# Kernel tuning notes

Measured on AMD Instinct MI355X. Metric: run time of the kernel, lower is better.

Reference implementation:

```python
import jax, jax.numpy as jnp
import numpy as np

# Multi-scale ball-query config (PFE.SA_LAYER.raw_points)
RADII = (0.8, 1.6)
NSAMPLES = (16, 32)
PC_SCALE = jnp.array([40.0, 40.0, 4.0])  # spread points over a realistic lidar extent


def _fps(pts, num_keypoints):
    """Furthest point sampling. pts: [N,3] -> idx [K] (int32). First pick = 0."""
    n = pts.shape[0]

    def step(carry, _):
        dists, last = carry
        d = jnp.sum((pts - pts[last]) ** 2, axis=-1)
        dists = jnp.minimum(dists, d)
        nxt = jnp.argmax(dists).astype(jnp.int32)
        return (dists, nxt), last

    init = (jnp.full((n,), 1e10, pts.dtype), jnp.int32(0))
    _, idxs = jax.lax.scan(step, init, None, length=num_keypoints)
    return idxs


def _glorot(k, shape):
    return jax.random.normal(k, shape) * (2.0 / (shape[0] + shape[1])) ** 0.5


def setup_inputs() -> dict:
    key = jax.random.key(0)
    ks = jax.random.split(key, 8)
    B, N = 2, 16384
    xyz = jax.random.uniform(ks[0], (B, N, 3)) * PC_SCALE          # [B,N,3]
    feat = jax.random.normal(ks[1], (B, 1, N))                      # intensity channel
    clouds = jnp.concatenate([xyz.transpose(0, 2, 1), feat], axis=1)  # [B,4,N]
    return {
        "clouds": clouds,
        "w1_a": _glorot(ks[2], (4, 128)),
        "w2_a": _glorot(ks[3], (128, 256)),
        "w1_b": _glorot(ks[4], (4, 128)),
        "w2_b": _glorot(ks[5], (128, 256)),
        "w_fuse": _glorot(ks[6], (512, 128)),
        "num_keypoints": 4096,
    }


def reference(clouds, w1_a, w2_a, w1_b, w2_b, w_fuse, num_keypoints):
    # clouds: [B, 4, N] with channels [x, y, z, intensity]
    xyz = clouds[:, :3, :].transpose(0, 2, 1)    # [B,N,3]
    feats = clouds[:, 3:, :].transpose(0, 2, 1)  # [B,N,1]

    # --- FPS keypoint sampling (per cloud) ---
    kp_idx = jax.vmap(lambda p: _fps(p, num_keypoints))(xyz)             # [B,K]
    keypoints = jnp.take_along_axis(xyz, kp_idx[:, :, None], axis=1)     # [B,K,3]

    # --- pairwise squared distances keypoints->points, shared by all scales ---
    d2 = jnp.sum((keypoints[:, :, None, :] - xyz[:, None, :, :]) ** 2, axis=-1)  # [B,K,N]

    gather = jax.vmap(lambda x, i: x[i])  # [N,C],[K,ns] -> [K,ns,C]

    pooled = []
    for r, ns, W1, W2 in ((RADII[0], NSAMPLES[0], w1_a, w2_a),
                          (RADII[1], NSAMPLES[1], w1_b, w2_b)):
        neg, idx = jax.lax.top_k(-d2, ns)            # ns nearest neighbors
        valid = (-neg) < (r * r)                     # [B,K,ns] within ball radius
        g_xyz = gather(xyz, idx) - keypoints[:, :, None, :]   # [B,K,ns,3] relative coords
        g_f = gather(feats, idx)                              # [B,K,ns,1]
        g = jnp.concatenate([g_xyz, g_f], axis=-1)            # [B,K,ns,4] (use_xyz=True)
        h = jax.nn.relu(jax.nn.relu(g @ W1) @ W2)             # shared PointNet MLP
        h = jnp.where(valid[..., None], h, 0.0)               # mask out-of-ball (relu>=0)
        pooled.append(jnp.max(h, axis=2))                     # max_pool -> [B,K,256]

    fused = jax.nn.relu(jnp.concatenate(pooled, axis=-1) @ w_fuse)  # [B,K,128]
    return jnp.concatenate([keypoints, fused], axis=-1)             # [B,K,3+128]
```

## Files before the change

### kernel.cpp

```cpp
#include <hip/hip_runtime.h>

typedef unsigned int u32;
typedef unsigned long long u64;
typedef float v2f __attribute__((ext_vector_type(2)));

__device__ __forceinline__ u64 shflx64(u64 v, int m) {
  int lo = __shfl_xor((int)(u32)v, m, 64);
  int hi = __shfl_xor((int)(u32)(v >> 32), m, 64);
  return ((u64)(u32)hi << 32) | (u32)lo;
}
__device__ __forceinline__ u64 maxu64(u64 a, u64 b) { return a > b ? a : b; }

template <int CTRL>
__device__ __forceinline__ u64 dpp_max64(u64 k) {
  int slo = __builtin_amdgcn_update_dpp(0, (int)(u32)k, CTRL, 0xF, 0xF, true);
  int shi = __builtin_amdgcn_update_dpp(0, (int)(u32)(k >> 32), CTRL, 0xF, 0xF, true);
  u64 s = ((u64)(u32)shi << 32) | (u32)slo;
  return maxu64(k, s);
}

__device__ __forceinline__ u64 row_max64(u64 k) {
  k = dpp_max64<0xB1>(k);
  k = dpp_max64<0x4E>(k);
  k = dpp_max64<0x124>(k);
  k = dpp_max64<0x128>(k);
  return k;
}

__device__ __forceinline__ float boxlb(float cx, float cy, float cz,
                                       float nx, float xx, float ny, float xy,
                                       float nz, float xz) {
  float gx = fmaxf(fmaxf(nx - cx, cx - xx), 0.0f);
  float gy = fmaxf(fmaxf(ny - cy, cy - xy), 0.0f);
  float gz = fmaxf(fmaxf(nz - cz, cz - xz), 0.0f);
  return gx * gx + gy * gy + gz * gz;
}

#define SORT_T 1024

__global__ __launch_bounds__(SORT_T) void k_sort(const float* __restrict__ clouds,
                                                 u32* __restrict__ order,
                                                 u32* __restrict__ bends,
                                                 float* __restrict__ meta, int N) {
  const int b = blockIdx.x, tid = threadIdx.x;
  const float* xs = clouds + (size_t)b * 4 * N;
  const float* ys = xs + N;
  const float* zs = ys + N;

  __shared__ u32 hist[2048];
  __shared__ u32 base[2048];
  __shared__ float red[96];
  __shared__ u32 wsum[16];

  float mnx = 3.4e38f, mxx = -3.4e38f, mny = 3.4e38f, mxy = -3.4e38f,
        mnz = 3.4e38f, mxz = -3.4e38f;
  for (int i = tid; i < N; i += SORT_T) {
    float x = xs[i], y = ys[i], z = zs[i];
    mnx = fminf(mnx, x); mxx = fmaxf(mxx, x);
    mny = fminf(mny, y); mxy = fmaxf(mxy, y);
    mnz = fminf(mnz, z); mxz = fmaxf(mxz, z);
  }
#pragma unroll
  for (int s = 1; s < 64; s <<= 1) {
    mnx = fminf(mnx, __shfl_xor(mnx, s, 64)); mxx = fmaxf(mxx, __shfl_xor(mxx, s, 64));
    mny = fminf(mny, __shfl_xor(mny, s, 64)); mxy = fmaxf(mxy, __shfl_xor(mxy, s, 64));
    mnz = fminf(mnz, __shfl_xor(mnz, s, 64)); mxz = fmaxf(mxz, __shfl_xor(mxz, s, 64));
  }
  const int wv = tid >> 6, ln = tid & 63;
  if (ln == 0) {
    red[wv * 6 + 0] = mnx; red[wv * 6 + 1] = mxx;
    red[wv * 6 + 2] = mny; red[wv * 6 + 3] = mxy;
    red[wv * 6 + 4] = mnz; red[wv * 6 + 5] = mxz;
  }
  hist[tid] = 0u; hist[tid + 1024] = 0u;
  __syncthreads();
  float bmnx = red[0], bmxx = red[1], bmny = red[2], bmxy = red[3],
        bmnz = red[4], bmxz = red[5];
// ... 35 lines not shown
  for (int d = 1; d < 64; d <<= 1) {
    u32 o = (u32)__shfl_up((int)x, d, 64);
    if (ln >= d) x += o;
  }
  if (ln == 63) wsum[wv] = x;
  __syncthreads();
  u32 wpre = 0;
#pragma unroll
  for (int w = 0; w < 16; ++w) wpre += (w < wv) ? wsum[w] : 0u;
  u32 tbase = wpre + x - ts;
  base[2 * tid] = tbase;
  base[2 * tid + 1] = tbase + s0;
  __syncthreads();

  for (int i = tid; i < N; i += SORT_T) {
    int qx = min(15, max(0, (int)((xs[i] - bmnx) * sx)));
    int qy = min(15, max(0, (int)((ys[i] - bmny) * sy)));
    int qz = min(7, max(0, (int)((zs[i] - bmnz) * sz)));
    u32 m = 0; int sh = 0;
#pragma unroll
    for (int bit = 0; bit < 4; ++bit) {
      m |= ((u32)((qx >> bit) & 1)) << sh++;
      m |= ((u32)((qy >> bit) & 1)) << sh++;
      if (bit < 3) m |= ((u32)((qz >> bit) & 1)) << sh++;
    }
    u32 pos = atomicAdd(&base[m], 1u);
    order[(size_t)b * N + pos] = (u32)i;
  }
  __syncthreads();
  for (int m = tid; m < 2048; m += SORT_T)
    bends[(size_t)b * 2048 + m] = base[m];
}

#define FPS_T 1024

__global__ __launch_bounds__(FPS_T, 4) void k_fps(const float* __restrict__ clouds,
                                                  const u32* __restrict__ order,
                                                  float* __restrict__ keyp,
                                                  int N, int K) {
  const int b = blockIdx.x, tid = threadIdx.x;
  const float* xs = clouds + (size_t)b * 4 * N;
  const float* ys = xs + N;
  const float* zs = ys + N;

  int oid[16];
  v2f px2[8], py2[8], pz2[8], dd2[8];
#pragma unroll
  for (int j = 0; j < 16; ++j) oid[j] = (int)order[(size_t)b * N + tid * 16 + j];
#pragma unroll
  for (int i = 0; i < 8; ++i) {
    px2[i].x = xs[oid[2 * i]]; px2[i].y = xs[oid[2 * i + 1]];
    py2[i].x = ys[oid[2 * i]]; py2[i].y = ys[oid[2 * i + 1]];
    pz2[i].x = zs[oid[2 * i]]; pz2[i].y = zs[oid[2 * i + 1]];
    dd2[i].x = 1e10f; dd2[i].y = 1e10f;
  }
  float bnx = px2[0].x, bxx = px2[0].x, bny = py2[0].x, bxy = py2[0].x,
        bnz = pz2[0].x, bxz = pz2[0].x;
#pragma unroll
  for (int i = 0; i < 8; ++i) {
    bnx = fminf(bnx, fminf(px2[i].x, px2[i].y));
    bxx = fmaxf(bxx, fmaxf(px2[i].x, px2[i].y));
    bny = fminf(bny, fminf(py2[i].x, py2[i].y));
    bxy = fmaxf(bxy, fmaxf(py2[i].x, py2[i].y));
    bnz = fminf(bnz, fminf(pz2[i].x, pz2[i].y));
    bxz = fmaxf(bxz, fmaxf(pz2[i].x, pz2[i].y));
  }
  float rnx = bnx, rxx = bxx, rny = bny, rxy = bxy, rnz = bnz, rxz = bxz;
#pragma unroll
  for (int s = 1; s < 16; s <<= 1) {
    rnx = fminf(rnx, __shfl_xor(rnx, s, 64)); rxx = fmaxf(rxx, __shfl_xor(rxx, s, 64));
    rny = fminf(rny, __shfl_xor(rny, s, 64)); rxy = fmaxf(rxy, __shfl_xor(rxy, s, 64));
    rnz = fminf(rnz, __shfl_xor(rnz, s, 64)); rxz = fmaxf(rxz, __shfl_xor(rxz, s, 64));
  }

  __shared__ u64 slots[2][64];
  const int wv = tid >> 6, ln = tid & 63;
  const int row = wv * 4 + (ln >> 4);
  const int q = ln & 15;

  u64 ckey = 0, rkey = 0;
  float cmax = 1e10f, rmax = 1e10f;
  float cx = xs[0], cy = ys[0], cz = zs[0];
  if (tid == 0) {
    float* kb = keyp + (size_t)b * K * 3;
    kb[0] = cx; kb[1] = cy; kb[2] = cz;
  }

  for (int t = 1; t < K; ++t) {
    const int par = t & 1;
    float gx = fmaxf(fmaxf(rnx - cx, cx - rxx), 0.0f);
    float gy = fmaxf(fmaxf(rny - cy, cy - rxy), 0.0f);
    float gz = fmaxf(fmaxf(rnz - cz, cz - rxz), 0.0f);
    float lbr = gx * gx + gy * gy + gz * gz;
    if (lbr <= rmax * 1.00001f) {
      float hx = fmaxf(fmaxf(bnx - cx, cx - bxx), 0.0f);
      float hy = fmaxf(fmaxf(bny - cy, cy - bxy), 0.0f);
      float hz = fmaxf(fmaxf(bnz - cz, cz - bxz), 0.0f);
      float lbt = hx * hx + hy * hy + hz * hz;
      if (lbt <= cmax * 1.00001f) {
        v2f m2 = {0.0f, 0.0f};
        {
#pragma clang fp contract(off)
          const v2f c2x = {cx, cx}, c2y = {cy, cy}, c2z = {cz, cz};
#pragma unroll
          for (int i = 0; i < 8; ++i) {
            v2f dx = px2[i] - c2x;
            v2f dy = py2[i] - c2y;
            v2f dz = pz2[i] - c2z;
            v2f d = (dx * dx + dy * dy) + dz * dz;
            v2f nm = __builtin_elementwise_min(dd2[i], d);
            dd2[i] = nm;
            m2 = __builtin_elementwise_max(m2, nm);
          }
        }
        const float m = fmaxf(m2.x, m2.y);
        u32 mi = 0xFFFFFFFFu;
#pragma unroll
        for (int i = 0; i < 8; ++i) {
          if (dd2[i].x == m) mi = min(mi, (u32)oid[2 * i]);
          if (dd2[i].y == m) mi = min(mi, (u32)oid[2 * i + 1]);
        }
        cmax = m;
        ckey = ((u64)__float_as_uint(m) << 32) | (u64)(u32)(~mi);
      }
      rkey = row_max64(ckey);
      rmax = __uint_as_float((u32)(rkey >> 32));
    }
    if (q == 0) slots[par][row] = rkey;
    __syncthreads();
    u64 k0 = slots[par][q];
    u64 k1 = slots[par][q + 16];
    u64 k2 = slots[par][q + 32];
    u64 k3 = slots[par][q + 48];
    u64 g = maxu64(maxu64(k0, k1), maxu64(k2, k3));
    g = row_max64(g);
    const u32 widx = __builtin_amdgcn_readfirstlane(~(u32)g);
    cx = xs[widx]; cy = ys[widx]; cz = zs[widx];
    if (tid == 0) {
      float* kb = keyp + ((size_t)b * K + t) * 3;
      kb[0] = cx; kb[1] = cy; kb[2] = cz;
    }
  }
}

#define KNN_T 256
#define KNN_CAP 1024
#define SENTINEL (((u64)0x7F7FFFFFu) << 32)

__global__ __launch_bounds__(KNN_T) void k_knn(const float* __restrict__ clouds,
                                               const float* __restrict__ keyp,
                                               const u32* __restrict__ order,
                                               const u32* __restrict__ bends,
                                               const float* __restrict__ meta,
                                               u64* __restrict__ slots,
                                               float* __restrict__ out,
                                               int N, int K, float r2b) {
  const int kp = blockIdx.x;
  const int b = kp / K;
  const int tid = threadIdx.x;
  const float* xs = clouds + (size_t)b * 4 * N;
  const float* ys = xs + N;
  const float* zs = ys + N;

  __shared__ u64 cand[KNN_CAP];
  __shared__ u32 lends[2048];
  __shared__ u32 blist[2048];
  __shared__ int cnt, bcnt;
  __shared__ u64 sorted32[32];

  if (tid == 0) { cnt = 0; bcnt = 0; }
  if (tid < 32) sorted32[tid] = SENTINEL;
  for (int m = tid; m < 2048; m += KNN_T) lends[m] = bends[(size_t)b * 2048 + m];
  const float kx = keyp[(size_t)kp * 3 + 0];
  const float ky = keyp[(size_t)kp * 3 + 1];
  const float kz = keyp[(size_t)kp * 3 + 2];
  const float bmnx = meta[b * 8 + 0], bmny = meta[b * 8 + 1], bmnz = meta[b * 8 + 2];
  const float csx = meta[b * 8 + 3], csy = meta[b * 8 + 4], csz = meta[b * 8 + 5];
  __syncthreads();

  for (int m = tid; m < 2048; m += KNN_T) {
    u32 qx = (m & 1) | ((m >> 2) & 2) | ((m >> 4) & 4) | ((m >> 6) & 8);
    u32 qy = ((m >> 1) & 1) | ((m >> 3) & 2) | ((m >> 5) & 4) | ((m >> 7) & 8);
    u32 qz = ((m >> 2) & 1) | ((m >> 4) & 2) | ((m >> 6) & 4);
    float lx = bmnx + (float)qx * csx - 1e-3f, hx = bmnx + (float)(qx + 1) * csx + 1e-3f;
    float ly = bmny + (float)qy * csy - 1e-3f, hy = bmny + (float)(qy + 1) * csy + 1e-3f;
    float lz = bmnz + (float)qz * csz - 1e-3f, hz = bmnz + (float)(qz + 1) * csz + 1e-3f;
    if (boxlb(kx, ky, kz, lx, hx, ly, hy, lz, hz) < r2b) {
      u32 s = m ? lends[m - 1] : 0u;
      u32 e = lends[m];
      if (e > s) {
        int p = atomicAdd(&bcnt, 1);
        blist[p] = s | (e << 16);
      }
    }
  }
  __syncthreads();

  const int nb = bcnt;
  for (int bi = 0; bi < nb; ++bi) {
    u32 pk = blist[bi];
    u32 s = pk & 0xFFFFu, e = pk >> 16;
    for (u32 i = s + tid; i < e; i += KNN_T) {
      u32 pi = order[(size_t)b * N + i];
      float dx = __fsub_rn(xs[pi], kx), dy = __fsub_rn(ys[pi], ky),
            dz = __fsub_rn(zs[pi], kz);
      float d = __fadd_rn(__fadd_rn(__fmul_rn(dx, dx), __fmul_rn(dy, dy)),
                          __fmul_rn(dz, dz));
      if (d < r2b) {
        int p = atomicAdd(&cnt, 1);
        if (p < KNN_CAP)
          cand[p] = (((u64)__float_as_uint(d)) << 32) | (u64)pi;
      }
    }
  }
  __syncthreads();
  int n = min(cnt, KNN_CAP);
  for (int i = tid; i < n; i += KNN_T) {
    u64 kk = cand[i];
    int r = 0;
    for (int j = 0; j < n; ++j) r += (cand[j] < kk) ? 1 : 0;
    if (r < 32) sorted32[r] = kk;
  }
  __syncthreads();
  if (tid < 32) slots[(size_t)kp * 32 + tid] = sorted32[tid];
  if (tid < 3) out[(size_t)kp * 131 + tid] = keyp[(size_t)kp * 3 + tid];
}

template <int M>
__global__ __launch_bounds__(256) void k_pool(const float* __restrict__ clouds,
                                              const float* __restrict__ keyp,
                                              const u64* __restrict__ slots,
                                              const float* __restrict__ w1,
                                              const float* __restrict__ w2,
                                              float* __restrict__ pooled,
                                              int N, int K, float R2, int colOff) {
  constexpr int R = M / 4;
  const int kp = blockIdx.x;
  const int b = kp / K;
  const int tid = threadIdx.x;
  const float* xs = clouds + (size_t)b * 4 * N;
  const float* ys = xs + N;
  const float* zs = ys + N;
  const float* fs = zs + N;

  __shared__ float w1l[512];
  __shared__ float gx[32], gy[32], gz[32], gf[32];
  __shared__ float h1l[32 * 132];
  __shared__ float w2l[32 * 256];
  __shared__ u32 pm[256];

  const float kx = keyp[(size_t)kp * 3 + 0];
  const float ky = keyp[(size_t)kp * 3 + 1];
  const float kz = keyp[(size_t)kp * 3 + 2];

  w1l[tid] = w1[tid];
  w1l[tid + 256] = w1[tid + 256];
  pm[tid] = 0u;
  if (tid < M) {
    u64 sl = slots[(size_t)kp * 32 + tid];
    float d2 = __uint_as_float((u32)(sl >> 32));
    u32 idx = (u32)sl;
    float vx = 0.f, vy = 0.f, vz = 0.f, vf = 0.f;
    if (d2 < R2) {
      vx = xs[idx] - kx;
      vy = ys[idx] - ky;
      vz = zs[idx] - kz;
      vf = fs[idx];
    }
    gx[tid] = vx; gy[tid] = vy; gz[tid] = vz; gf[tid] = vf;
  }
  __syncthreads();

  {
    const int c = tid & 127;
#pragma unroll
    for (int p = 0; p < M / 2; ++p) {
      int r = p * 2 + (tid >> 7);
      float h = fmaf(gf[r], w1l[384 + c],
                fmaf(gz[r], w1l[256 + c],
                fmaf(gy[r], w1l[128 + c], gx[r] * w1l[c])));
      h1l[r * 132 + c] = fmaxf(h, 0.0f);
    }
  }

  const int rt = tid >> 6;
  const int cg = tid & 63;
  float acc[R][4];
#pragma unroll
  for (int rr = 0; rr < R; ++rr)
#pragma unroll
    for (int cc = 0; cc < 4; ++cc) acc[rr][cc] = 0.0f;

  for (int kt = 0; kt < 4; ++kt) {
    __syncthreads();
    for (int q = tid; q < 32 * 256; q += 256)
      w2l[q] = w2[(size_t)(kt * 32 + (q >> 8)) * 256 + (q & 255)];
    __syncthreads();
    for (int k = 0; k < 32; k += 4) {
      float4 hv[R];
#pragma unroll
      for (int rr = 0; rr < R; ++rr)
        hv[rr] = *reinterpret_cast<const float4*>(
            &h1l[(rt * R + rr) * 132 + kt * 32 + k]);
      float4 wv[4];
#pragma unroll
      for (int kk = 0; kk < 4; ++kk)
        wv[kk] = *reinterpret_cast<const float4*>(
            &w2l[(k + kk) * 256 + cg * 4]);
#pragma unroll
      for (int rr = 0; rr < R; ++rr) {
        const float a0 = hv[rr].x, a1 = hv[rr].y, a2 = hv[rr].z, a3 = hv[rr].w;
        acc[rr][0] = fmaf(a3, wv[3].x, fmaf(a2, wv[2].x,
                     fmaf(a1, wv[1].x, fmaf(a0, wv[0].x, acc[rr][0]))));
        acc[rr][1] = fmaf(a3, wv[3].y, fmaf(a2, wv[2].y,
                     fmaf(a1, wv[1].y, fmaf(a0, wv[0].y, acc[rr][1]))));
        acc[rr][2] = fmaf(a3, wv[3].z, fmaf(a2, wv[2].z,
                     fmaf(a1, wv[1].z, fmaf(a0, wv[0].z, acc[rr][2]))));
        acc[rr][3] = fmaf(a3, wv[3].w, fmaf(a2, wv[2].w,
                     fmaf(a1, wv[1].w, fmaf(a0, wv[0].w, acc[rr][3]))));
      }
    }
  }
#pragma unroll
  for (int cc = 0; cc < 4; ++cc) {
    float mx = 0.0f;
#pragma unroll
    for (int rr = 0; rr < R; ++rr) mx = fmaxf(mx, acc[rr][cc]);
    atomicMax(&pm[cg * 4 + cc], __float_as_uint(mx));
  }
  __syncthreads();
  pooled[(size_t)kp * 512 + colOff + tid] = __uint_as_float(pm[tid]);
}

__global__ __launch_bounds__(256) void k_fuse(const float* __restrict__ pooled,
                                              const float* __restrict__ wf,
                                              float* __restrict__ out) {
  const int m0 = blockIdx.x * 16;
  const int tid = threadIdx.x;
  __shared__ float al[16 * 516];
  __shared__ float wl[32 * 128];

  for (int q = tid; q < 16 * 512; q += 256)
    al[(q >> 9) * 516 + (q & 511)] =
        pooled[(size_t)(m0 + (q >> 9)) * 512 + (q & 511)];

  const int rg = tid >> 5;
  const int cg = tid & 31;
  float acc[2][4];
#pragma unroll
  for (int rr = 0; rr < 2; ++rr)
#pragma unroll
    for (int cc = 0; cc < 4; ++cc) acc[rr][cc] = 0.0f;

  for (int kt = 0; kt < 16; ++kt) {
    __syncthreads();
    for (int q = tid; q < 32 * 128; q += 256)
      wl[q] = wf[(size_t)(kt * 32 + (q >> 7)) * 128 + (q & 127)];
    __syncthreads();
    for (int k = 0; k < 32; k += 4) {
      float4 av[2];
#pragma unroll
      for (int rr = 0; rr < 2; ++rr)
        av[rr] = *reinterpret_cast<const float4*>(
            &al[(rg * 2 + rr) * 516 + kt * 32 + k]);
// ... 22 lines not shown
    for (int cc = 0; cc < 4; ++cc)
      out[row * 131 + 3 + cg * 4 + cc] = fmaxf(acc[rr][cc], 0.0f);
  }
}

extern "C" void kernel_launch(void* const* d_in, const int* in_sizes, int n_in,
                              void* d_out, int out_size, void* d_ws, size_t ws_size,
                              hipStream_t stream) {
  const float* clouds = (const float*)d_in[0];
  const float* w1a = (const float*)d_in[1];
  const float* w2a = (const float*)d_in[2];
  const float* w1b = (const float*)d_in[3];
  const float* w2b = (const float*)d_in[4];
  const float* wfu = (const float*)d_in[5];
  float* out = (float*)d_out;

  const int B = 2;
  const int N = in_sizes[0] / (4 * B);
  const int K = out_size / (131 * B);
  const int BK = B * K;

  char* ws = (char*)d_ws;
  u32* order = (u32*)ws;
  size_t off = ((size_t)B * N * sizeof(u32) + 255) & ~(size_t)255;
  u32* bends = (u32*)(ws + off);
  off += (size_t)B * 2048 * sizeof(u32);
  off = (off + 255) & ~(size_t)255;
  float* meta = (float*)(ws + off);
  off += (size_t)B * 8 * sizeof(float);
  off = (off + 255) & ~(size_t)255;
  float* keyp = (float*)(ws + off);
  off += (size_t)BK * 3 * sizeof(float);
  off = (off + 255) & ~(size_t)255;
  u64* slots = (u64*)(ws + off);
  off += (size_t)BK * 32 * sizeof(u64);
  off = (off + 255) & ~(size_t)255;
  float* pooled = (float*)(ws + off);

  const float r2a = (float)(0.8 * 0.8);
  const float r2b = (float)(1.6 * 1.6);

  k_sort<<<dim3(B), dim3(SORT_T), 0, stream>>>(clouds, order, bends, meta, N);
  k_fps<<<dim3(B), dim3(FPS_T), 0, stream>>>(clouds, order, keyp, N, K);
  k_knn<<<dim3(BK), dim3(KNN_T), 0, stream>>>(clouds, keyp, order, bends, meta,
                                              slots, out, N, K, r2b);
  k_pool<16><<<dim3(BK), dim3(256), 0, stream>>>(clouds, keyp, slots, w1a, w2a,
                                                 pooled, N, K, r2a, 0);
  k_pool<32><<<dim3(BK), dim3(256), 0, stream>>>(clouds, keyp, slots, w1b, w2b,
                                                 pooled, N, K, r2b, 256);
  k_fuse<<<dim3(BK / 16), dim3(256), 0, stream>>>(pooled, wfu, out);
}
```

Measured before the change: 4.400 ms.

## Overlap FPS with KNN and pooling in a persistent megakernel with progress flags

FPS, KNN and both pooling stages now run in one persistent kernel. Two blocks run FPS and publish keypoints in batches of 64 along with a per-cloud progress counter. The other blocks pull chunks of keypoints through an atomic work counter, spin until each keypoint is published, then run ball-query KNN and both PointNet MLPs back to back in shared memory. This hides the sequential FPS latency behind the downstream work and removes the intermediate slots buffer and two launches. The costs are spin-wait polling, co-residency assumptions for the FPS blocks, and 1024-thread worker blocks where many threads sit idle in the 256-wide MLP stages.

```diff
diff --git a/kernel.cpp b/kernel.cpp
--- a/kernel.cpp
+++ b/kernel.cpp
@@ -4,11 +4,6 @@
 typedef unsigned long long u64;
 typedef float v2f __attribute__((ext_vector_type(2)));
 
-__device__ __forceinline__ u64 shflx64(u64 v, int m) {
-  int lo = __shfl_xor((int)(u32)v, m, 64);
-  int hi = __shfl_xor((int)(u32)(v >> 32), m, 64);
-  return ((u64)(u32)hi << 32) | (u32)lo;
-}
 __device__ __forceinline__ u64 maxu64(u64 a, u64 b) { return a > b ? a : b; }
 
 template <int CTRL>
@@ -18,7 +13,6 @@
   u64 s = ((u64)(u32)shi << 32) | (u32)slo;
   return maxu64(k, s);
 }
-
 __device__ __forceinline__ u64 row_max64(u64 k) {
   k = dpp_max64<0xB1>(k);
   k = dpp_max64<0x4E>(k);
@@ -41,8 +35,10 @@
 __global__ __launch_bounds__(SORT_T) void k_sort(const float* __restrict__ clouds,
                                                  u32* __restrict__ order,
                                                  u32* __restrict__ bends,
-                                                 float* __restrict__ meta, int N) {
+                                                 float* __restrict__ meta,
+                                                 u32* prog, int N) {
   const int b = blockIdx.x, tid = threadIdx.x;
+  if (b == 0 && tid == 0) { prog[0] = 0u; prog[1] = 0u; prog[2] = 0u; }
   const float* xs = clouds + (size_t)b * 4 * N;
   const float* ys = xs + N;
   const float* zs = ys + N;
@@ -144,12 +140,16 @@
     bends[(size_t)b * 2048 + m] = base[m];
 }
 
-#define FPS_T 1024
-
-__global__ __launch_bounds__(FPS_T, 4) void k_fps(const float* __restrict__ clouds,
-                                                  const u32* __restrict__ order,
-                                                  float* __restrict__ keyp,
-                                                  int N, int K) {
+#define KNN_CAP 1024
+#define SENTINEL (((u64)0x7F7FFFFFu) << 32)
+#define CHUNK 4
+#define MEGA_T 1024
+
+#define SM_BYTES 37376
+
+__device__ void fps_body(const float* __restrict__ clouds,
+                         const u32* __restrict__ order,
+                         float* keyp, u32* prog, int N, int K, char* smemc) {
   const int b = blockIdx.x, tid = threadIdx.x;
   const float* xs = clouds + (size_t)b * 4 * N;
   const float* ys = xs + N;
@@ -185,7 +185,7 @@
     rnz = fminf(rnz, __shfl_xor(rnz, s, 64)); rxz = fmaxf(rxz, __shfl_xor(rxz, s, 64));
   }
 
-  __shared__ u64 slots[2][64];
+  u64 (*slots)[64] = (u64 (*)[64])smemc;
   const int wv = tid >> 6, ln = tid & 63;
   const int row = wv * 4 + (ln >> 4);
   const int q = ln & 15;
@@ -193,10 +193,7 @@
   u64 ckey = 0, rkey = 0;
   float cmax = 1e10f, rmax = 1e10f;
   float cx = xs[0], cy = ys[0], cz = zs[0];
-  if (tid == 0) {
-    float* kb = keyp + (size_t)b * K * 3;
-    kb[0] = cx; kb[1] = cy; kb[2] = cz;
-  }
+  float bpx = cx, bpy = cy, bpz = cz;
 
   for (int t = 1; t < K; ++t) {
     const int par = t & 1;
@@ -248,128 +245,48 @@
     g = row_max64(g);
     const u32 widx = __builtin_amdgcn_readfirstlane(~(u32)g);
     cx = xs[widx]; cy = ys[widx]; cz = zs[widx];
-    if (tid == 0) {
-      float* kb = keyp + ((size_t)b * K + t) * 3;
-      kb[0] = cx; kb[1] = cy; kb[2] = cz;
-    }
-  }
-}
-
-#define KNN_T 256
-#define KNN_CAP 1024
-#define SENTINEL (((u64)0x7F7FFFFFu) << 32)
-
-__global__ __launch_bounds__(KNN_T) void k_knn(const float* __restrict__ clouds,
-                                               const float* __restrict__ keyp,
-                                               const u32* __restrict__ order,
-                                               const u32* __restrict__ bends,
-                                               const float* __restrict__ meta,
-                                               u64* __restrict__ slots,
-                                               float* __restrict__ out,
-                                               int N, int K, float r2b) {
-  const int kp = blockIdx.x;
-  const int b = kp / K;
-  const int tid = threadIdx.x;
-  const float* xs = clouds + (size_t)b * 4 * N;
-  const float* ys = xs + N;
-  const float* zs = ys + N;
-
-  __shared__ u64 cand[KNN_CAP];
-  __shared__ u32 lends[2048];
-  __shared__ u32 blist[2048];
-  __shared__ int cnt, bcnt;
-  __shared__ u64 sorted32[32];
-
-  if (tid == 0) { cnt = 0; bcnt = 0; }
-  if (tid < 32) sorted32[tid] = SENTINEL;
-  for (int m = tid; m < 2048; m += KNN_T) lends[m] = bends[(size_t)b * 2048 + m];
-  const float kx = keyp[(size_t)kp * 3 + 0];
-  const float ky = keyp[(size_t)kp * 3 + 1];
-  const float kz = keyp[(size_t)kp * 3 + 2];
-  const float bmnx = meta[b * 8 + 0], bmny = meta[b * 8 + 1], bmnz = meta[b * 8 + 2];
-  const float csx = meta[b * 8 + 3], csy = meta[b * 8 + 4], csz = meta[b * 8 + 5];
-  __syncthreads();
-
-  for (int m = tid; m < 2048; m += KNN_T) {
-    u32 qx = (m & 1) | ((m >> 2) & 2) | ((m >> 4) & 4) | ((m >> 6) & 8);
-    u32 qy = ((m >> 1) & 1) | ((m >> 3) & 2) | ((m >> 5) & 4) | ((m >> 7) & 8);
-    u32 qz = ((m >> 2) & 1) | ((m >> 4) & 2) | ((m >> 6) & 4);
-    float lx = bmnx + (float)qx * csx - 1e-3f, hx = bmnx + (float)(qx + 1) * csx + 1e-3f;
-    float ly = bmny + (float)qy * csy - 1e-3f, hy = bmny + (float)(qy + 1) * csy + 1e-3f;
-    float lz = bmnz + (float)qz * csz - 1e-3f, hz = bmnz + (float)(qz + 1) * csz + 1e-3f;
-    if (boxlb(kx, ky, kz, lx, hx, ly, hy, lz, hz) < r2b) {
-      u32 s = m ? lends[m - 1] : 0u;
-      u32 e = lends[m];
-      if (e > s) {
-        int p = atomicAdd(&bcnt, 1);
-        blist[p] = s | (e << 16);
-      }
-    }
-  }
-  __syncthreads();
-
-  const int nb = bcnt;
-  for (int bi = 0; bi < nb; ++bi) {
-    u32 pk = blist[bi];
-    u32 s = pk & 0xFFFFu, e = pk >> 16;
-    for (u32 i = s + tid; i < e; i += KNN_T) {
-      u32 pi = order[(size_t)b * N + i];
-      float dx = __fsub_rn(xs[pi], kx), dy = __fsub_rn(ys[pi], ky),
-            dz = __fsub_rn(zs[pi], kz);
-      float d = __fadd_rn(__fadd_rn(__fmul_rn(dx, dx), __fmul_rn(dy, dy)),
-                          __fmul_rn(dz, dz));
-      if (d < r2b) {
-        int p = atomicAdd(&cnt, 1);
-        if (p < KNN_CAP)
-          cand[p] = (((u64)__float_as_uint(d)) << 32) | (u64)pi;
-      }
-    }
-  }
-  __syncthreads();
-  int n = min(cnt, KNN_CAP);
-  for (int i = tid; i < n; i += KNN_T) {
-    u64 kk = cand[i];
-    int r = 0;
-    for (int j = 0; j < n; ++j) r += (cand[j] < kk) ? 1 : 0;
-    if (r < 32) sorted32[r] = kk;
-  }
-  __syncthreads();
-  if (tid < 32) slots[(size_t)kp * 32 + tid] = sorted32[tid];
-  if (tid < 3) out[(size_t)kp * 131 + tid] = keyp[(size_t)kp * 3 + tid];
+    if (wv == 0) {
+      if (ln == (t & 63)) { bpx = cx; bpy = cy; bpz = cz; }
+      if ((t & 63) == 63) {
+        u32* kb = (u32*)keyp + ((size_t)b * K + (size_t)(t - 63 + ln)) * 3;
+        __hip_atomic_store(kb + 0, __float_as_uint(bpx), __ATOMIC_RELAXED, __HIP_MEMORY_SCOPE_AGENT);
+        __hip_atomic_store(kb + 1, __float_as_uint(bpy), __ATOMIC_RELAXED, __HIP_MEMORY_SCOPE_AGENT);
+        __hip_atomic_store(kb + 2, __float_as_uint(bpz), __ATOMIC_RELAXED, __HIP_MEMORY_SCOPE_AGENT);
+        asm volatile("s_waitcnt vmcnt(0)" ::: "memory");
+        if (ln == 0)
+          __hip_atomic_store(prog + b, (u32)(t + 1), __ATOMIC_RELAXED, __HIP_MEMORY_SCOPE_AGENT);
+      }
+    }
+  }
+  if ((K & 63) != 0 && wv == 0) {
+    int base = (K - 1) & ~63;
+    int kpt = base + ln;
+    if (kpt < K && ln <= ((K - 1) & 63)) {
+      u32* kb = (u32*)keyp + ((size_t)b * K + (size_t)kpt) * 3;
+      __hip_atomic_store(kb + 0, __float_as_uint(bpx), __ATOMIC_RELAXED, __HIP_MEMORY_SCOPE_AGENT);
+      __hip_atomic_store(kb + 1, __float_as_uint(bpy), __ATOMIC_RELAXED, __HIP_MEMORY_SCOPE_AGENT);
+      __hip_atomic_store(kb + 2, __float_as_uint(bpz), __ATOMIC_RELAXED, __HIP_MEMORY_SCOPE_AGENT);
+    }
+    asm volatile("s_waitcnt vmcnt(0)" ::: "memory");
+    if (ln == 0)
+      __hip_atomic_store(prog + b, (u32)K, __ATOMIC_RELAXED, __HIP_MEMORY_SCOPE_AGENT);
+  }
 }
 
 template <int M>
-__global__ __launch_bounds__(256) void k_pool(const float* __restrict__ clouds,
-                                              const float* __restrict__ keyp,
-                                              const u64* __restrict__ slots,
-                                              const float* __restrict__ w1,
-                                              const float* __restrict__ w2,
-                                              float* __restrict__ pooled,
-                                              int N, int K, float R2, int colOff) {
+__device__ void pool_stage(const float* xs, const float* ys, const float* zs,
+                           const float* fs, float kx, float ky, float kz,
+                           const u64* s32, const float* __restrict__ w1,
+                           const float* __restrict__ w2, float* pooled, int kp,
+                           float R2, int colOff, float* w1l, float* gxa,
+                           float* gya, float* gza, float* gfa, float* h1l,
+                           float* w2l, u32* pm, int tid) {
   constexpr int R = M / 4;
-  const int kp = blockIdx.x;
-  const int b = kp / K;
-  const int tid = threadIdx.x;
-  const float* xs = clouds + (size_t)b * 4 * N;
-  const float* ys = xs + N;
-  const float* zs = ys + N;
-  const float* fs = zs + N;
-
-  __shared__ float w1l[512];
-  __shared__ float gx[32], gy[32], gz[32], gf[32];
-  __shared__ float h1l[32 * 132];
-  __shared__ float w2l[32 * 256];
-  __shared__ u32 pm[256];
-
-  const float kx = keyp[(size_t)kp * 3 + 0];
-  const float ky = keyp[(size_t)kp * 3 + 1];
-  const float kz = keyp[(size_t)kp * 3 + 2];
-
-  w1l[tid] = w1[tid];
-  w1l[tid + 256] = w1[tid + 256];
-  pm[tid] = 0u;
+  __syncthreads();
+  if (tid < 512) w1l[tid] = w1[tid];
+  if (tid < 256) pm[tid] = 0u;
   if (tid < M) {
-    u64 sl = slots[(size_t)kp * 32 + tid];
+    u64 sl = s32[tid];
     float d2 = __uint_as_float((u32)(sl >> 32));
     u32 idx = (u32)sl;
     float vx = 0.f, vy = 0.f, vz = 0.f, vf = 0.f;
@@ -379,23 +296,23 @@
       vz = zs[idx] - kz;
       vf = fs[idx];
     }
-    gx[tid] = vx; gy[tid] = vy; gz[tid] = vz; gf[tid] = vf;
-  }
-  __syncthreads();
-
-  {
+    gxa[tid] = vx; gya[tid] = vy; gza[tid] = vz; gfa[tid] = vf;
+  }
+  __syncthreads();
+
+  if (tid < 256) {
     const int c = tid & 127;
 #pragma unroll
     for (int p = 0; p < M / 2; ++p) {
       int r = p * 2 + (tid >> 7);
-      float h = fmaf(gf[r], w1l[384 + c],
-                fmaf(gz[r], w1l[256 + c],
-                fmaf(gy[r], w1l[128 + c], gx[r] * w1l[c])));
+      float h = fmaf(gfa[r], w1l[384 + c],
+                fmaf(gza[r], w1l[256 + c],
+                fmaf(gya[r], w1l[128 + c], gxa[r] * w1l[c])));
       h1l[r * 132 + c] = fmaxf(h, 0.0f);
     }
   }
 
-  const int rt = tid >> 6;
+  const int rt = (tid & 255) >> 6;
   const int cg = tid & 63;
   float acc[R][4];
 #pragma unroll
@@ -403,45 +320,177 @@
 #pragma unroll
     for (int cc = 0; cc < 4; ++cc) acc[rr][cc] = 0.0f;
 
-  for (int kt = 0; kt < 4; ++kt) {
+  for (int kt = 0; kt < 8; ++kt) {
     __syncthreads();
-    for (int q = tid; q < 32 * 256; q += 256)
-      w2l[q] = w2[(size_t)(kt * 32 + (q >> 8)) * 256 + (q & 255)];
+    for (int q2 = tid; q2 < 16 * 256; q2 += MEGA_T)
+      w2l[q2] = w2[(size_t)(kt * 16 + (q2 >> 8)) * 256 + (q2 & 255)];
     __syncthreads();
-    for (int k = 0; k < 32; k += 4) {
-      float4 hv[R];
-#pragma unroll
-      for (int rr = 0; rr < R; ++rr)
-        hv[rr] = *reinterpret_cast<const float4*>(
-            &h1l[(rt * R + rr) * 132 + kt * 32 + k]);
-      float4 wv[4];
-#pragma unroll
-      for (int kk = 0; kk < 4; ++kk)
-        wv[kk] = *reinterpret_cast<const float4*>(
-            &w2l[(k + kk) * 256 + cg * 4]);
-#pragma unroll
-      for (int rr = 0; rr < R; ++rr) {
-        const float a0 = hv[rr].x, a1 = hv[rr].y, a2 = hv[rr].z, a3 = hv[rr].w;
-        acc[rr][0] = fmaf(a3, wv[3].x, fmaf(a2, wv[2].x,
-                     fmaf(a1, wv[1].x, fmaf(a0, wv[0].x, acc[rr][0]))));
-        acc[rr][1] = fmaf(a3, wv[3].y, fmaf(a2, wv[2].y,
-                     fmaf(a1, wv[1].y, fmaf(a0, wv[0].y, acc[rr][1]))));
-        acc[rr][2] = fmaf(a3, wv[3].z, fmaf(a2, wv[2].z,
-                     fmaf(a1, wv[1].z, fmaf(a0, wv[0].z, acc[rr][2]))));
-        acc[rr][3] = fmaf(a3, wv[3].w, fmaf(a2, wv[2].w,
-                     fmaf(a1, wv[1].w, fmaf(a0, wv[0].w, acc[rr][3]))));
-      }
-    }
-  }
-#pragma unroll
-  for (int cc = 0; cc < 4; ++cc) {
-    float mx = 0.0f;
-#pragma unroll
-    for (int rr = 0; rr < R; ++rr) mx = fmaxf(mx, acc[rr][cc]);
-    atomicMax(&pm[cg * 4 + cc], __float_as_uint(mx));
-  }
-  __syncthreads();
-  pooled[(size_t)kp * 512 + colOff + tid] = __uint_as_float(pm[tid]);
+    if (tid < 256) {
+      for (int k = 0; k < 16; k += 4) {
+        float4 hv[R];
+#pragma unroll
+        for (int rr = 0; rr < R; ++rr)
+          hv[rr] = *reinterpret_cast<const float4*>(
+              &h1l[(rt * R + rr) * 132 + kt * 16 + k]);
+        float4 wv[4];
+#pragma unroll
+        for (int kk = 0; kk < 4; ++kk)
+          wv[kk] = *reinterpret_cast<const float4*>(
+              &w2l[(k + kk) * 256 + cg * 4]);
+#pragma unroll
+        for (int rr = 0; rr < R; ++rr) {
+          const float a0 = hv[rr].x, a1 = hv[rr].y, a2 = hv[rr].z, a3 = hv[rr].w;
+          acc[rr][0] = fmaf(a3, wv[3].x, fmaf(a2, wv[2].x,
+                       fmaf(a1, wv[1].x, fmaf(a0, wv[0].x, acc[rr][0]))));
+          acc[rr][1] = fmaf(a3, wv[3].y, fmaf(a2, wv[2].y,
+                       fmaf(a1, wv[1].y, fmaf(a0, wv[0].y, acc[rr][1]))));
+          acc[rr][2] = fmaf(a3, wv[3].z, fmaf(a2, wv[2].z,
+                       fmaf(a1, wv[1].z, fmaf(a0, wv[0].z, acc[rr][2]))));
+          acc[rr][3] = fmaf(a3, wv[3].w, fmaf(a2, wv[2].w,
+                       fmaf(a1, wv[1].w, fmaf(a0, wv[0].w, acc[rr][3]))));
+        }
+      }
+    }
+  }
+  if (tid < 256) {
+#pragma unroll
+    for (int cc = 0; cc < 4; ++cc) {
+      float mx = 0.0f;
+#pragma unroll
+      for (int rr = 0; rr < R; ++rr) mx = fmaxf(mx, acc[rr][cc]);
+      atomicMax(&pm[cg * 4 + cc], __float_as_uint(mx));
+    }
+  }
+  __syncthreads();
+  if (tid < 256)
+    pooled[(size_t)kp * 512 + colOff + tid] = __uint_as_float(pm[tid]);
+}
+
+__device__ void worker_body(const float* __restrict__ clouds,
+                            const float* keyp, const u32* __restrict__ order,
+                            const u32* __restrict__ bends,
+                            const float* __restrict__ meta,
+                            const float* __restrict__ w1a, const float* __restrict__ w2a,
+                            const float* __restrict__ w1b, const float* __restrict__ w2b,
+                            float* pooled, float* out, u32* prog, int N, int K,
+                            char* smem) {
+  const int tid = threadIdx.x;
+  u64* cand  = (u64*)(smem);
+  u32* lends = (u32*)(smem + 8192);
+  u32* blist = (u32*)(smem + 16384);
+  int* cnt   = (int*)(smem + 24576);
+  int* bcnt  = (int*)(smem + 24580);
+  float* w1l = (float*)(smem);
+  float* gxa = (float*)(smem + 2048);
+  float* gya = (float*)(smem + 2176);
+  float* gza = (float*)(smem + 2304);
+  float* gfa = (float*)(smem + 2432);
+  float* h1l = (float*)(smem + 2560);
+  float* w2l = (float*)(smem + 19456);
+  u32* pm    = (u32*)(smem + 35840);
+  u64* s32   = (u64*)(smem + 36864);
+  volatile int* shc = (int*)(smem + 37120);
+
+  const int nch = (2 * K) / CHUNK;
+  for (;;) {
+    if (tid == 0) *shc = (int)atomicAdd(prog + 2, 1u);
+    __syncthreads();
+    const int c = *shc;
+    if (c >= nch) break;
+    for (int j = 0; j < CHUNK; ++j) {
+      const int kp = c * CHUNK + j;
+      const int b = kp / K;
+      const int t = kp - b * K;
+      if (tid == 0) {
+        while (__hip_atomic_load(prog + b, __ATOMIC_ACQUIRE,
+                                 __HIP_MEMORY_SCOPE_AGENT) < (u32)(t + 1))
+          __builtin_amdgcn_s_sleep(32);
+      }
+      __syncthreads();
+
+      const float* xs = clouds + (size_t)b * 4 * N;
+      const float* ys = xs + N;
+      const float* zs = ys + N;
+      const float* fs = zs + N;
+
+      if (tid == 0) { *cnt = 0; *bcnt = 0; }
+      if (tid < 32) s32[tid] = SENTINEL;
+      for (int m = tid; m < 2048; m += MEGA_T)
+        lends[m] = bends[(size_t)b * 2048 + m];
+      const float kx = keyp[(size_t)kp * 3 + 0];
+      const float ky = keyp[(size_t)kp * 3 + 1];
+      const float kz = keyp[(size_t)kp * 3 + 2];
+      const float bmnx = meta[b * 8 + 0], bmny = meta[b * 8 + 1], bmnz = meta[b * 8 + 2];
+      const float csx = meta[b * 8 + 3], csy = meta[b * 8 + 4], csz = meta[b * 8 + 5];
+      const float r2b = 2.56f;
+      __syncthreads();
+
+      for (int m = tid; m < 2048; m += MEGA_T) {
+        u32 qx = (m & 1) | ((m >> 2) & 2) | ((m >> 4) & 4) | ((m >> 6) & 8);
+        u32 qy = ((m >> 1) & 1) | ((m >> 3) & 2) | ((m >> 5) & 4) | ((m >> 7) & 8);
+        u32 qz = ((m >> 2) & 1) | ((m >> 4) & 2) | ((m >> 6) & 4);
+        float lx = bmnx + (float)qx * csx - 1e-3f, hx = bmnx + (float)(qx + 1) * csx + 1e-3f;
+        float ly = bmny + (float)qy * csy - 1e-3f, hy = bmny + (float)(qy + 1) * csy + 1e-3f;
+        float lz = bmnz + (float)qz * csz - 1e-3f, hz = bmnz + (float)(qz + 1) * csz + 1e-3f;
+        if (boxlb(kx, ky, kz, lx, hx, ly, hy, lz, hz) < r2b) {
+          u32 s = m ? lends[m - 1] : 0u;
+          u32 e = lends[m];
+          if (e > s) {
+            int p = atomicAdd(bcnt, 1);
+            blist[p] = s | (e << 16);
+          }
+        }
+      }
+      __syncthreads();
+
+      const int nb = *bcnt;
+      for (int bi = 0; bi < nb; ++bi) {
+        u32 pk = blist[bi];
+        u32 s = pk & 0xFFFFu, e = pk >> 16;
+        for (u32 i = s + tid; i < e; i += MEGA_T) {
+          u32 pi = order[(size_t)b * N + i];
+          float dx = __fsub_rn(xs[pi], kx), dy = __fsub_rn(ys[pi], ky),
+                dz = __fsub_rn(zs[pi], kz);
+          float d = __fadd_rn(__fadd_rn(__fmul_rn(dx, dx), __fmul_rn(dy, dy)),
+                              __fmul_rn(dz, dz));
+          if (d < r2b) {
+            int p = atomicAdd(cnt, 1);
+            if (p < KNN_CAP)
+              cand[p] = (((u64)__float_as_uint(d)) << 32) | (u64)pi;
+          }
+        }
+      }
+      __syncthreads();
+      int n = min(*cnt, KNN_CAP);
+      for (int i = tid; i < n; i += MEGA_T) {
+        u64 kk = cand[i];
+        int r = 0;
+        for (int jj = 0; jj < n; ++jj) r += (cand[jj] < kk) ? 1 : 0;
+        if (r < 32) s32[r] = kk;
+      }
+      __syncthreads();
+      if (tid < 3) out[(size_t)kp * 131 + tid] = keyp[(size_t)kp * 3 + tid];
+
+      pool_stage<16>(xs, ys, zs, fs, kx, ky, kz, s32, w1a, w2a, pooled, kp,
+                     0.64f, 0, w1l, gxa, gya, gza, gfa, h1l, w2l, pm, tid);
+      pool_stage<32>(xs, ys, zs, fs, kx, ky, kz, s32, w1b, w2b, pooled, kp,
+                     2.56f, 256, w1l, gxa, gya, gza, gfa, h1l, w2l, pm, tid);
+    }
+  }
+}
+
+__global__ __launch_bounds__(MEGA_T, 4) void k_mega(
+    const float* __restrict__ clouds, const u32* __restrict__ order,
+    const u32* __restrict__ bends, const float* __restrict__ meta,
+    float* keyp, const float* __restrict__ w1a, const float* __restrict__ w2a,
+    const float* __restrict__ w1b, const float* __restrict__ w2b,
+    float* pooled, float* out, u32* prog, int N, int K) {
+  __shared__ __align__(16) char smem[SM_BYTES];
+  if (blockIdx.x < 2)
+    fps_body(clouds, order, keyp, prog, N, K, smem);
+  else
+    worker_body(clouds, keyp, order, bends, meta, w1a, w2a, w1b, w2b, pooled,
+                out, prog, N, K, smem);
 }
 
 __global__ __launch_bounds__(256) void k_fuse(const float* __restrict__ pooled,
@@ -530,21 +579,14 @@
   float* keyp = (float*)(ws + off);
   off += (size_t)BK * 3 * sizeof(float);
   off = (off + 255) & ~(size_t)255;
-  u64* slots = (u64*)(ws + off);
-  off += (size_t)BK * 32 * sizeof(u64);
+  float* pooled = (float*)(ws + off);
+  off += (size_t)BK * 512 * sizeof(float);
   off = (off + 255) & ~(size_t)255;
-  float* pooled = (float*)(ws + off);
-
-  const float r2a = (float)(0.8 * 0.8);
-  const float r2b = (float)(1.6 * 1.6);
-
-  k_sort<<<dim3(B), dim3(SORT_T), 0, stream>>>(clouds, order, bends, meta, N);
-  k_fps<<<dim3(B), dim3(FPS_T), 0, stream>>>(clouds, order, keyp, N, K);
-  k_knn<<<dim3(BK), dim3(KNN_T), 0, stream>>>(clouds, keyp, order, bends, meta,
-                                              slots, out, N, K, r2b);
-  k_pool<16><<<dim3(BK), dim3(256), 0, stream>>>(clouds, keyp, slots, w1a, w2a,
-                                                 pooled, N, K, r2a, 0);
-  k_pool<32><<<dim3(BK), dim3(256), 0, stream>>>(clouds, keyp, slots, w1b, w2b,
-                                                 pooled, N, K, r2b, 256);
+  u32* prog = (u32*)(ws + off);
+
+  k_sort<<<dim3(B), dim3(SORT_T), 0, stream>>>(clouds, order, bends, meta, prog, N);
+  k_mega<<<dim3(256), dim3(MEGA_T), 0, stream>>>(clouds, order, bends, meta,
+                                                 keyp, w1a, w2a, w1b, w2b,
+                                                 pooled, out, prog, N, K);
   k_fuse<<<dim3(BK / 16), dim3(256), 0, stream>>>(pooled, wfu, out);
 }
```

New measurement: 6.115 ms. +39.0%, slower.

## Fuse kNN ball query with both pooling MLPs and skip out-of-ball rows

Applied to the files above, without the earlier changes.

Merges the kNN kernel and both per-scale PointNet pooling kernels into one per-keypoint kernel that reuses an aliased shared-memory buffer. This removes the global slot round trip and two launches. It also counts the neighbours inside each radius and skips layer-1 and layer-2 MLP work for rows beyond that count, since masked rows contribute zero to the max. W2 is now read directly from global memory instead of being staged in shared memory, which may raise global/cache traffic per block.

```diff
diff --git a/kernel.cpp b/kernel.cpp
--- a/kernel.cpp
+++ b/kernel.cpp
@@ -4,11 +4,6 @@
 typedef unsigned long long u64;
 typedef float v2f __attribute__((ext_vector_type(2)));
 
-__device__ __forceinline__ u64 shflx64(u64 v, int m) {
-  int lo = __shfl_xor((int)(u32)v, m, 64);
-  int hi = __shfl_xor((int)(u32)(v >> 32), m, 64);
-  return ((u64)(u32)hi << 32) | (u32)lo;
-}
 __device__ __forceinline__ u64 maxu64(u64 a, u64 b) { return a > b ? a : b; }
 
 template <int CTRL>
@@ -18,7 +13,6 @@
   u64 s = ((u64)(u32)shi << 32) | (u32)slo;
   return maxu64(k, s);
 }
-
 __device__ __forceinline__ u64 row_max64(u64 k) {
   k = dpp_max64<0xB1>(k);
   k = dpp_max64<0x4E>(k);
@@ -255,34 +249,131 @@
   }
 }
 
-#define KNN_T 256
+#define BP_T 256
 #define KNN_CAP 1024
 #define SENTINEL (((u64)0x7F7FFFFFu) << 32)
 
-__global__ __launch_bounds__(KNN_T) void k_knn(const float* __restrict__ clouds,
-                                               const float* __restrict__ keyp,
-                                               const u32* __restrict__ order,
-                                               const u32* __restrict__ bends,
-                                               const float* __restrict__ meta,
-                                               u64* __restrict__ slots,
-                                               float* __restrict__ out,
-                                               int N, int K, float r2b) {
+template <int M>
+__device__ __forceinline__ void pool_scale(
+    const float* xs, const float* ys, const float* zs, const float* fs,
+    float kx, float ky, float kz, float R2, const float* __restrict__ w1,
+    const float* __restrict__ w2, float* __restrict__ pooled, int kp,
+    int colOff, const int* vp, const u64* s32, float* w1l, float* gxa,
+    float* gya, float* gza, float* gfa, float* h1l, u32* pm, int tid) {
+  constexpr int R = M / 4;
+  w1l[tid] = w1[tid];
+  w1l[tid + 256] = w1[tid + 256];
+  pm[tid] = 0u;
+  if (tid < M) {
+    u64 sl = s32[tid];
+    float d2 = __uint_as_float((u32)(sl >> 32));
+    u32 idx = (u32)sl;
+    float vx = 0.f, vy = 0.f, vz = 0.f, vf = 0.f;
+    if (d2 < R2) {
+      vx = xs[idx] - kx;
+      vy = ys[idx] - ky;
+      vz = zs[idx] - kz;
+      vf = fs[idx];
+    }
+    gxa[tid] = vx; gya[tid] = vy; gza[tid] = vz; gfa[tid] = vf;
+  }
+  __syncthreads();
+  const int v = min(*vp, M);
+
+  {
+    const int c = tid & 127;
+#pragma unroll
+    for (int p = 0; p < M / 2; ++p) {
+      int r = p * 2 + (tid >> 7);
+      if (r < v) {
+        float h = fmaf(gfa[r], w1l[384 + c],
+                  fmaf(gza[r], w1l[256 + c],
+                  fmaf(gya[r], w1l[128 + c], gxa[r] * w1l[c])));
+        h1l[r * 132 + c] = fmaxf(h, 0.0f);
+      }
+    }
+  }
+  __syncthreads();
+
+  const int rt = tid >> 6;
+  const int cg = tid & 63;
+  const int rbase = rt * R;
+  const int rlim = min(R, max(0, v - rbase));
+  float acc[R][4];
+#pragma unroll
+  for (int rr = 0; rr < R; ++rr)
+#pragma unroll
+    for (int cc = 0; cc < 4; ++cc) acc[rr][cc] = 0.0f;
+
+  if (rlim > 0) {
+    for (int k = 0; k < 128; k += 4) {
+      float4 wv[4];
+#pragma unroll
+      for (int kk = 0; kk < 4; ++kk)
+        wv[kk] = *reinterpret_cast<const float4*>(&w2[(size_t)(k + kk) * 256 + cg * 4]);
+#pragma unroll
+      for (int rr = 0; rr < R; ++rr) {
+        if (rr < rlim) {
+          float4 hv = *reinterpret_cast<const float4*>(&h1l[(rbase + rr) * 132 + k]);
+          const float a0 = hv.x, a1 = hv.y, a2 = hv.z, a3 = hv.w;
+          acc[rr][0] = fmaf(a3, wv[3].x, fmaf(a2, wv[2].x,
+                       fmaf(a1, wv[1].x, fmaf(a0, wv[0].x, acc[rr][0]))));
+          acc[rr][1] = fmaf(a3, wv[3].y, fmaf(a2, wv[2].y,
+                       fmaf(a1, wv[1].y, fmaf(a0, wv[0].y, acc[rr][1]))));
+          acc[rr][2] = fmaf(a3, wv[3].z, fmaf(a2, wv[2].z,
+                       fmaf(a1, wv[1].z, fmaf(a0, wv[0].z, acc[rr][2]))));
+          acc[rr][3] = fmaf(a3, wv[3].w, fmaf(a2, wv[2].w,
+                       fmaf(a1, wv[1].w, fmaf(a0, wv[0].w, acc[rr][3]))));
+        }
+      }
+    }
+#pragma unroll
+    for (int cc = 0; cc < 4; ++cc) {
+      float mx = 0.0f;
+#pragma unroll
+      for (int rr = 0; rr < R; ++rr) mx = fmaxf(mx, acc[rr][cc]);
+      atomicMax(&pm[cg * 4 + cc], __float_as_uint(mx));
+    }
+  }
+  __syncthreads();
+  pooled[(size_t)kp * 512 + colOff + tid] = __uint_as_float(pm[tid]);
+}
+
+__global__ __launch_bounds__(BP_T) void k_ballpool(
+    const float* __restrict__ clouds, const float* __restrict__ keyp,
+    const u32* __restrict__ order, const u32* __restrict__ bends,
+    const float* __restrict__ meta, const float* __restrict__ w1a,
+    const float* __restrict__ w2a, const float* __restrict__ w1b,
+    const float* __restrict__ w2b, float* __restrict__ pooled,
+    float* __restrict__ out, int N, int K) {
   const int kp = blockIdx.x;
   const int b = kp / K;
   const int tid = threadIdx.x;
   const float* xs = clouds + (size_t)b * 4 * N;
   const float* ys = xs + N;
   const float* zs = ys + N;
-
-  __shared__ u64 cand[KNN_CAP];
-  __shared__ u32 lends[2048];
-  __shared__ u32 blist[2048];
-  __shared__ int cnt, bcnt;
-  __shared__ u64 sorted32[32];
-
-  if (tid == 0) { cnt = 0; bcnt = 0; }
-  if (tid < 32) sorted32[tid] = SENTINEL;
-  for (int m = tid; m < 2048; m += KNN_T) lends[m] = bends[(size_t)b * 2048 + m];
+  const float* fs = zs + N;
+
+  __shared__ __align__(16) char sm[24576];
+  __shared__ u64 s32[32];
+  __shared__ int scnt[4];
+
+  u64* cand  = (u64*)sm;
+  u32* lends = (u32*)(sm + 8192);
+  u32* blist = (u32*)(sm + 16384);
+  float* w1l = (float*)sm;
+  float* gxa = (float*)(sm + 2048);
+  float* gya = (float*)(sm + 2176);
+  float* gza = (float*)(sm + 2304);
+  float* gfa = (float*)(sm + 2432);
+  float* h1l = (float*)(sm + 2560);
+  u32* pm    = (u32*)(sm + 19456);
+
+  const float r2a = 0.64f, r2b = 2.56f;
+
+  if (tid == 0) { scnt[0] = 0; scnt[1] = 0; }
+  if (tid < 32) s32[tid] = SENTINEL;
+  for (int m = tid; m < 2048; m += BP_T) lends[m] = bends[(size_t)b * 2048 + m];
   const float kx = keyp[(size_t)kp * 3 + 0];
   const float ky = keyp[(size_t)kp * 3 + 1];
   const float kz = keyp[(size_t)kp * 3 + 2];
@@ -290,7 +381,7 @@
   const float csx = meta[b * 8 + 3], csy = meta[b * 8 + 4], csz = meta[b * 8 + 5];
   __syncthreads();
 
-  for (int m = tid; m < 2048; m += KNN_T) {
+  for (int m = tid; m < 2048; m += BP_T) {
     u32 qx = (m & 1) | ((m >> 2) & 2) | ((m >> 4) & 4) | ((m >> 6) & 8);
     u32 qy = ((m >> 1) & 1) | ((m >> 3) & 2) | ((m >> 5) & 4) | ((m >> 7) & 8);
     u32 qz = ((m >> 2) & 1) | ((m >> 4) & 2) | ((m >> 6) & 4);
@@ -301,147 +392,53 @@
       u32 s = m ? lends[m - 1] : 0u;
       u32 e = lends[m];
       if (e > s) {
-        int p = atomicAdd(&bcnt, 1);
+        int p = atomicAdd(&scnt[1], 1);
         blist[p] = s | (e << 16);
       }
     }
   }
   __syncthreads();
 
-  const int nb = bcnt;
+  const int nb = scnt[1];
   for (int bi = 0; bi < nb; ++bi) {
     u32 pk = blist[bi];
     u32 s = pk & 0xFFFFu, e = pk >> 16;
-    for (u32 i = s + tid; i < e; i += KNN_T) {
+    for (u32 i = s + tid; i < e; i += BP_T) {
       u32 pi = order[(size_t)b * N + i];
       float dx = __fsub_rn(xs[pi], kx), dy = __fsub_rn(ys[pi], ky),
             dz = __fsub_rn(zs[pi], kz);
       float d = __fadd_rn(__fadd_rn(__fmul_rn(dx, dx), __fmul_rn(dy, dy)),
                           __fmul_rn(dz, dz));
       if (d < r2b) {
-        int p = atomicAdd(&cnt, 1);
+        int p = atomicAdd(&scnt[0], 1);
         if (p < KNN_CAP)
           cand[p] = (((u64)__float_as_uint(d)) << 32) | (u64)pi;
       }
     }
   }
   __syncthreads();
-  int n = min(cnt, KNN_CAP);
-  for (int i = tid; i < n; i += KNN_T) {
+  int n = min(scnt[0], KNN_CAP);
+  for (int i = tid; i < n; i += BP_T) {
     u64 kk = cand[i];
     int r = 0;
     for (int j = 0; j < n; ++j) r += (cand[j] < kk) ? 1 : 0;
-    if (r < 32) sorted32[r] = kk;
-  }
-  __syncthreads();
-  if (tid < 32) slots[(size_t)kp * 32 + tid] = sorted32[tid];
+    if (r < 32) s32[r] = kk;
+  }
+  __syncthreads();
+
+  if (tid < 64) {
+    bool oka = (tid < 32) && (__uint_as_float((u32)(s32[tid] >> 32)) < r2a);
+    bool okb = (tid < 32) && (__uint_as_float((u32)(s32[tid] >> 32)) < r2b);
+    u64 ma = __ballot(oka);
+    u64 mb = __ballot(okb);
+    if (tid == 0) { scnt[2] = (int)__popcll(ma); scnt[3] = (int)__popcll(mb); }
+  }
   if (tid < 3) out[(size_t)kp * 131 + tid] = keyp[(size_t)kp * 3 + tid];
-}
-
-template <int M>
-__global__ __launch_bounds__(256) void k_pool(const float* __restrict__ clouds,
-                                              const float* __restrict__ keyp,
-                                              const u64* __restrict__ slots,
-                                              const float* __restrict__ w1,
-                                              const float* __restrict__ w2,
-                                              float* __restrict__ pooled,
-                                              int N, int K, float R2, int colOff) {
-  constexpr int R = M / 4;
-  const int kp = blockIdx.x;
-  const int b = kp / K;
-  const int tid = threadIdx.x;
-  const float* xs = clouds + (size_t)b * 4 * N;
-  const float* ys = xs + N;
-  const float* zs = ys + N;
-  const float* fs = zs + N;
-
-  __shared__ float w1l[512];
-  __shared__ float gx[32], gy[32], gz[32], gf[32];
-  __shared__ float h1l[32 * 132];
-  __shared__ float w2l[32 * 256];
-  __shared__ u32 pm[256];
-
-  const float kx = keyp[(size_t)kp * 3 + 0];
-  const float ky = keyp[(size_t)kp * 3 + 1];
-  const float kz = keyp[(size_t)kp * 3 + 2];
-
-  w1l[tid] = w1[tid];
-  w1l[tid + 256] = w1[tid + 256];
-  pm[tid] = 0u;
-  if (tid < M) {
-    u64 sl = slots[(size_t)kp * 32 + tid];
-    float d2 = __uint_as_float((u32)(sl >> 32));
-    u32 idx = (u32)sl;
-    float vx = 0.f, vy = 0.f, vz = 0.f, vf = 0.f;
-    if (d2 < R2) {
-      vx = xs[idx] - kx;
-      vy = ys[idx] - ky;
-      vz = zs[idx] - kz;
-      vf = fs[idx];
-    }
-    gx[tid] = vx; gy[tid] = vy; gz[tid] = vz; gf[tid] = vf;
-  }
-  __syncthreads();
-
-  {
-    const int c = tid & 127;
-#pragma unroll
-    for (int p = 0; p < M / 2; ++p) {
-      int r = p * 2 + (tid >> 7);
-      float h = fmaf(gf[r], w1l[384 + c],
-                fmaf(gz[r], w1l[256 + c],
-                fmaf(gy[r], w1l[128 + c], gx[r] * w1l[c])));
-      h1l[r * 132 + c] = fmaxf(h, 0.0f);
-    }
-  }
-
-  const int rt = tid >> 6;
-  const int cg = tid & 63;
-  float acc[R][4];
-#pragma unroll
-  for (int rr = 0; rr < R; ++rr)
-#pragma unroll
-    for (int cc = 0; cc < 4; ++cc) acc[rr][cc] = 0.0f;
-
-  for (int kt = 0; kt < 4; ++kt) {
-    __syncthreads();
-    for (int q = tid; q < 32 * 256; q += 256)
-      w2l[q] = w2[(size_t)(kt * 32 + (q >> 8)) * 256 + (q & 255)];
-    __syncthreads();
-    for (int k = 0; k < 32; k += 4) {
-      float4 hv[R];
-#pragma unroll
-      for (int rr = 0; rr < R; ++rr)
-        hv[rr] = *reinterpret_cast<const float4*>(
-            &h1l[(rt * R + rr) * 132 + kt * 32 + k]);
-      float4 wv[4];
-#pragma unroll
-      for (int kk = 0; kk < 4; ++kk)
-        wv[kk] = *reinterpret_cast<const float4*>(
-            &w2l[(k + kk) * 256 + cg * 4]);
-#pragma unroll
-      for (int rr = 0; rr < R; ++rr) {
-        const float a0 = hv[rr].x, a1 = hv[rr].y, a2 = hv[rr].z, a3 = hv[rr].w;
-        acc[rr][0] = fmaf(a3, wv[3].x, fmaf(a2, wv[2].x,
-                     fmaf(a1, wv[1].x, fmaf(a0, wv[0].x, acc[rr][0]))));
-        acc[rr][1] = fmaf(a3, wv[3].y, fmaf(a2, wv[2].y,
-                     fmaf(a1, wv[1].y, fmaf(a0, wv[0].y, acc[rr][1]))));
-        acc[rr][2] = fmaf(a3, wv[3].z, fmaf(a2, wv[2].z,
-                     fmaf(a1, wv[1].z, fmaf(a0, wv[0].z, acc[rr][2]))));
-        acc[rr][3] = fmaf(a3, wv[3].w, fmaf(a2, wv[2].w,
-                     fmaf(a1, wv[1].w, fmaf(a0, wv[0].w, acc[rr][3]))));
-      }
-    }
-  }
-#pragma unroll
-  for (int cc = 0; cc < 4; ++cc) {
-    float mx = 0.0f;
-#pragma unroll
-    for (int rr = 0; rr < R; ++rr) mx = fmaxf(mx, acc[rr][cc]);
-    atomicMax(&pm[cg * 4 + cc], __float_as_uint(mx));
-  }
-  __syncthreads();
-  pooled[(size_t)kp * 512 + colOff + tid] = __uint_as_float(pm[tid]);
+
+  pool_scale<16>(xs, ys, zs, fs, kx, ky, kz, r2a, w1a, w2a, pooled, kp, 0,
+                 &scnt[2], s32, w1l, gxa, gya, gza, gfa, h1l, pm, tid);
+  pool_scale<32>(xs, ys, zs, fs, kx, ky, kz, r2b, w1b, w2b, pooled, kp, 256,
+                 &scnt[3], s32, w1l, gxa, gya, gza, gfa, h1l, pm, tid);
 }
 
 __global__ __launch_bounds__(256) void k_fuse(const float* __restrict__ pooled,
@@ -530,21 +527,12 @@
   float* keyp = (float*)(ws + off);
   off += (size_t)BK * 3 * sizeof(float);
   off = (off + 255) & ~(size_t)255;
-  u64* slots = (u64*)(ws + off);
-  off += (size_t)BK * 32 * sizeof(u64);
-  off = (off + 255) & ~(size_t)255;
   float* pooled = (float*)(ws + off);
-
-  const float r2a = (float)(0.8 * 0.8);
-  const float r2b = (float)(1.6 * 1.6);
 
   k_sort<<<dim3(B), dim3(SORT_T), 0, stream>>>(clouds, order, bends, meta, N);
   k_fps<<<dim3(B), dim3(FPS_T), 0, stream>>>(clouds, order, keyp, N, K);
-  k_knn<<<dim3(BK), dim3(KNN_T), 0, stream>>>(clouds, keyp, order, bends, meta,
-                                              slots, out, N, K, r2b);
-  k_pool<16><<<dim3(BK), dim3(256), 0, stream>>>(clouds, keyp, slots, w1a, w2a,
-                                                 pooled, N, K, r2a, 0);
-  k_pool<32><<<dim3(BK), dim3(256), 0, stream>>>(clouds, keyp, slots, w1b, w2b,
-                                                 pooled, N, K, r2b, 256);
+  k_ballpool<<<dim3(BK), dim3(BP_T), 0, stream>>>(clouds, keyp, order, bends,
+                                                  meta, w1a, w2a, w1b, w2b,
+                                                  pooled, out, N, K);
   k_fuse<<<dim3(BK / 16), dim3(256), 0, stream>>>(pooled, wfu, out);
 }
```

After: 4.224 ms. -4.0%, faster.
